# Kernel tuning notes

Measured on AMD Instinct MI355X. Metric: run time of the kernel, lower is better.

## Reference

```python
import jax, jax.numpy as jnp
import numpy as np

N_NODES = 50000
N_EDGES = 800000
IN_CH = 256
OUT_CH = 64
HEADS = 4
NEG_SLOPE = 0.2


def setup_inputs() -> dict:
    key = jax.random.key(0)
    k = jax.random.split(key, 7)
    x = jax.random.normal(k[0], (N_NODES, IN_CH), dtype=jnp.float32)
    edge_index = jax.random.randint(k[1], (2, N_EDGES), 0, N_NODES, dtype=jnp.int32)
    # Glorot-style init for the linear projection and attention vectors
    W = jax.random.normal(k[2], (IN_CH, HEADS * OUT_CH), dtype=jnp.float32) / np.sqrt(IN_CH)
    att_src = jax.random.normal(k[3], (HEADS, OUT_CH), dtype=jnp.float32) / np.sqrt(OUT_CH)
    att_dst = jax.random.normal(k[4], (HEADS, OUT_CH), dtype=jnp.float32) / np.sqrt(OUT_CH)
    bias = jnp.zeros((HEADS * OUT_CH,), dtype=jnp.float32)
    return {"x": x, "edge_index": edge_index, "W": W,
            "att_src": att_src, "att_dst": att_dst, "bias": bias}


def reference(x, edge_index, W, att_src, att_dst, bias):
    N = x.shape[0]
    # PyG GATConv default: add self-loops
    loop = jnp.arange(N, dtype=edge_index.dtype)
    src = jnp.concatenate([edge_index[0], loop])
    dst = jnp.concatenate([edge_index[1], loop])

    h = (x @ W).reshape(N, HEADS, OUT_CH)          # [N,H,C]
    a_src = jnp.einsum('nhc,hc->nh', h, att_src)    # [N,H]
    a_dst = jnp.einsum('nhc,hc->nh', h, att_dst)    # [N,H]

    alpha = a_src[src] + a_dst[dst]                 # [E,H]
    alpha = jax.nn.leaky_relu(alpha, NEG_SLOPE)

    # segment softmax over edges grouped by destination node
    amax = jax.ops.segment_max(alpha, dst, num_segments=N)
    amax = jnp.where(jnp.isfinite(amax), amax, 0.0)
    e = jnp.exp(alpha - amax[dst])
    denom = jax.ops.segment_sum(e, dst, num_segments=N)
    coef = e / (denom[dst] + 1e-16)                 # [E,H]

    msg = coef[..., None] * h[src]                  # [E,H,C]
    out = jax.ops.segment_sum(msg, dst, num_segments=N)  # [N,H,C]
    out = out.reshape(N, HEADS * OUT_CH) + bias
    return jax.nn.relu(out)
```

## Files before the change

kernel.cpp:

```cpp
#include <hip/hip_runtime.h>

#define HC 256
#define NEG_SLOPE 0.2f
#define BM 64
#define BK 64
#define LDK 72

typedef short short8_t __attribute__((ext_vector_type(8)));
typedef float float4_t __attribute__((ext_vector_type(4)));

__device__ __forceinline__ unsigned short f2bf(float f) {
  unsigned u = __float_as_uint(f);
  return (unsigned short)((u + 0x7fffu + ((u >> 16) & 1u)) >> 16);
}
__device__ __forceinline__ float bf2f(unsigned short b) {
  return __uint_as_float(((unsigned)b) << 16);
}

__global__ void wt_kernel(const float* __restrict__ W, unsigned short* __restrict__ Wt)
{
  const int k = blockIdx.x;
  const int n = threadIdx.x;
  Wt[n * 256 + k] = f2bf(W[k * 256 + n]);
}

__global__ __launch_bounds__(256) void gemm_mfma(
    const float* __restrict__ x, const unsigned short* __restrict__ Wt,
    const float* __restrict__ att_src, const float* __restrict__ att_dst,
    unsigned short* __restrict__ h, float* __restrict__ a_src,
    float* __restrict__ a_dst, int nnodes)
{
  __shared__ unsigned short As[BM * LDK];
  __shared__ unsigned short Bs[256 * LDK];
  const int t    = threadIdx.x;
  const int wv   = t >> 6;
  const int lane = t & 63;
  const int r0   = blockIdx.x * BM;

  float4_t acc[4][4] = {};

  for (int k0 = 0; k0 < 256; k0 += BK) {
    __syncthreads();
    {
      const int row = t >> 2, kc = (t & 3) * 16;
      const int gr = r0 + row;
      float4 xv[4];
      if (gr < nnodes) {
        const float4* p = (const float4*)(x + (size_t)gr * 256 + k0 + kc);
        xv[0] = p[0]; xv[1] = p[1]; xv[2] = p[2]; xv[3] = p[3];
      } else {
        xv[0] = xv[1] = xv[2] = xv[3] = make_float4(0.f, 0.f, 0.f, 0.f);
      }
      const float* f = (const float*)xv;
      unsigned pk[8];
      #pragma unroll
      for (int i = 0; i < 8; ++i)
        pk[i] = (unsigned)f2bf(f[2 * i]) | ((unsigned)f2bf(f[2 * i + 1]) << 16);
      uint4* d = (uint4*)&As[row * LDK + kc];
      d[0] = make_uint4(pk[0], pk[1], pk[2], pk[3]);
      d[1] = make_uint4(pk[4], pk[5], pk[6], pk[7]);
    }
    #pragma unroll
    for (int it = 0; it < 4; ++it) {
      const int n = it * 64 + (t >> 2);
      const int kc = (t & 3) * 16;
      const uint4* g = (const uint4*)(Wt + (size_t)n * 256 + k0 + kc);
      uint4 v0 = g[0], v1 = g[1];
      uint4* d = (uint4*)&Bs[n * LDK + kc];
      d[0] = v0; d[1] = v1;
    }
    __syncthreads();

    #pragma unroll
    for (int ks = 0; ks < 2; ++ks) {
      const int ko = ks * 32 + (lane >> 4) * 8;
      short8_t af[4], bfr[4];
      #pragma unroll
      for (int mt = 0; mt < 4; ++mt)
        af[mt] = *(const short8_t*)&As[(16 * mt + (lane & 15)) * LDK + ko];
      #pragma unroll
      for (int nt = 0; nt < 4; ++nt)
        bfr[nt] = *(const short8_t*)&Bs[(64 * wv + 16 * nt + (lane & 15)) * LDK + ko];
      #pragma unroll
      for (int mt = 0; mt < 4; ++mt)
        #pragma unroll
        for (int nt = 0; nt < 4; ++nt)
          acc[mt][nt] = __builtin_amdgcn_mfma_f32_16x16x32_bf16(
              af[mt], bfr[nt], acc[mt][nt], 0, 0, 0);
    }
  }

  const int q = lane >> 4, l15 = lane & 15;
  float atts[4], attd[4];
  #pragma unroll
  for (int nt = 0; nt < 4; ++nt) {
    atts[nt] = att_src[wv * 64 + 16 * nt + l15];
    attd[nt] = att_dst[wv * 64 + 16 * nt + l15];
  }

  #pragma unroll
  for (int mt = 0; mt < 4; ++mt) {
    #pragma unroll
    for (int reg = 0; reg < 4; ++reg) {
      const int row = r0 + 16 * mt + 4 * q + reg;
      const bool ok = row < nnodes;
      float ps = 0.f, pd = 0.f;
      #pragma unroll
      for (int nt = 0; nt < 4; ++nt) {
        const float v = acc[mt][nt][reg];
        if (ok) h[(size_t)row * 256 + 64 * wv + 16 * nt + l15] = f2bf(v);
        ps += v * atts[nt];
        pd += v * attd[nt];
      }
      #pragma unroll
      for (int off = 8; off; off >>= 1) {
        ps += __shfl_down(ps, off, 16);
        pd += __shfl_down(pd, off, 16);
      }
      if (ok && l15 == 0) {
        a_src[row * 4 + wv] = ps;
        a_dst[row * 4 + wv] = pd;
      }
    }
  }
}

__global__ void deg_count(const int* __restrict__ ei, int* __restrict__ deg, int E)
{
  const int e = blockIdx.x * blockDim.x + threadIdx.x;
  if (e >= E) return;
  atomicAdd(&deg[ei[E + e]], 1);
}

__global__ __launch_bounds__(256) void scan_p1(const int* __restrict__ deg,
                                               int* __restrict__ bsum, int n)
{
  __shared__ int ws[4];
  const int t = threadIdx.x, lane = t & 63, wv = t >> 6;
  const int base = blockIdx.x * 1024 + t * 4;
  int4 v = make_int4(0, 0, 0, 0);
  if (base + 3 < n) v = *(const int4*)&deg[base];
  else {
    if (base + 0 < n) v.x = deg[base + 0];
    if (base + 1 < n) v.y = deg[base + 1];
    if (base + 2 < n) v.z = deg[base + 2];
  }
  int s = (v.x + v.y) + (v.z + v.w);
  #pragma unroll
  for (int off = 32; off; off >>= 1) s += __shfl_down(s, off, 64);
  if (lane == 0) ws[wv] = s;
  __syncthreads();
  if (t == 0) bsum[blockIdx.x] = (ws[0] + ws[1]) + (ws[2] + ws[3]);
}

__global__ __launch_bounds__(1024) void scan_p2(const int* __restrict__ bsum,
                                                int* __restrict__ boff,
                                                int* __restrict__ rowptr,
                                                int nb, int n)
{
  __shared__ int wsum[16], woff[16];
  const int t = threadIdx.x, lane = t & 63, wv = t >> 6;
  int v = (t < nb) ? bsum[t] : 0;
  int sc = v;
  #pragma unroll
  for (int off = 1; off < 64; off <<= 1) {
    int u = __shfl_up(sc, off, 64);
    if (lane >= off) sc += u;
  }
  if (lane == 63) wsum[wv] = sc;
  __syncthreads();
  if (t == 0) {
    int run = 0;
    #pragma unroll
    for (int i = 0; i < 16; ++i) { int x = wsum[i]; woff[i] = run; run += x; }
    rowptr[n] = run;
  }
  __syncthreads();
  if (t < nb) boff[t] = woff[wv] + sc - v;
}

__global__ __launch_bounds__(256) void scan_p3(const int* __restrict__ deg,
                                               const int* __restrict__ boff,
                                               int* __restrict__ rowptr,
                                               int* __restrict__ cursor, int n)
{
  __shared__ int wsum[4], woff[4];
  const int t = threadIdx.x, lane = t & 63, wv = t >> 6;
  const int base = blockIdx.x * 1024 + t * 4;
  int4 v = make_int4(0, 0, 0, 0);
  if (base + 3 < n) v = *(const int4*)&deg[base];
  else {
    if (base + 0 < n) v.x = deg[base + 0];
    if (base + 1 < n) v.y = deg[base + 1];
    if (base + 2 < n) v.z = deg[base + 2];
  }
  const int s = (v.x + v.y) + (v.z + v.w);
  int sc = s;
  #pragma unroll
  for (int off = 1; off < 64; off <<= 1) {
    int u = __shfl_up(sc, off, 64);
    if (lane >= off) sc += u;
  }
  if (lane == 63) wsum[wv] = sc;
  __syncthreads();
  if (t == 0) {
    int run = 0;
    #pragma unroll
    for (int i = 0; i < 4; ++i) { int x = wsum[i]; woff[i] = run; run += x; }
  }
  __syncthreads();
  int excl = boff[blockIdx.x] + woff[wv] + (sc - s);
  int4 r;
  r.x = excl;
  r.y = r.x + v.x;
  r.z = r.y + v.y;
  r.w = r.z + v.z;
  if (base + 3 < n) {
    *(int4*)&rowptr[base] = r;
    *(int4*)&cursor[base] = r;
  } else {
    if (base + 0 < n) { rowptr[base + 0] = r.x; cursor[base + 0] = r.x; }
    if (base + 1 < n) { rowptr[base + 1] = r.y; cursor[base + 1] = r.y; }
    if (base + 2 < n) { rowptr[base + 2] = r.z; cursor[base + 2] = r.z; }
  }
}

__global__ void fill_csr(const int* __restrict__ ei, int* __restrict__ cursor,
                         int* __restrict__ csr_src, int E)
{
  const int e = blockIdx.x * blockDim.x + threadIdx.x;
  if (e >= E) return;
  const int d = ei[E + e];
  const int pos = atomicAdd(&cursor[d], 1);
  csr_src[pos] = ei[e];
}

__device__ __forceinline__ float4 ld_h(const unsigned short* __restrict__ h,
                                       int row, int cb)
{
  const ushort4 u = *(const ushort4*)&h[(size_t)row * 256 + cb];
  return make_float4(bf2f(u.x), bf2f(u.y), bf2f(u.z), bf2f(u.w));
}

__global__ __launch_bounds__(256) void gather_kernel(
    const int* __restrict__ rowptr, const int* __restrict__ csr_src,
    const unsigned short* __restrict__ h, const float* __restrict__ a_src,
    const float* __restrict__ a_dst, const float* __restrict__ bias,
    float* __restrict__ out, int n)
{
  const int wave = threadIdx.x >> 6;
  const int lane = threadIdx.x & 63;
  const int d = blockIdx.x * 4 + wave;
  if (d >= n) return;

  const int head = lane >> 4;
  const int cb   = lane * 4;
  const float ad = a_dst[d * 4 + head];

  float alpha = a_src[d * 4 + head] + ad;
  alpha = alpha > 0.f ? alpha : NEG_SLOPE * alpha;
  float w = expf(alpha);
  float dsum = w;
  float4 hv = ld_h(h, d, cb);
  float4 acc = make_float4(w * hv.x, w * hv.y, w * hv.z, w * hv.w);

  int j = rowptr[d];
  const int end = rowptr[d + 1];

  for (; j + 3 < end; j += 4) {
    const int s0 = csr_src[j + 0];
    const int s1 = csr_src[j + 1];
    const int s2 = csr_src[j + 2];
    const int s3 = csr_src[j + 3];
    const float a0 = a_src[s0 * 4 + head];
    const float a1 = a_src[s1 * 4 + head];
    const float a2 = a_src[s2 * 4 + head];
    const float a3 = a_src[s3 * 4 + head];
    const float4 h0 = ld_h(h, s0, cb);
    const float4 h1 = ld_h(h, s1, cb);
    const float4 h2 = ld_h(h, s2, cb);
    const float4 h3 = ld_h(h, s3, cb);
    float l0 = a0 + ad; l0 = l0 > 0.f ? l0 : NEG_SLOPE * l0;
    float l1 = a1 + ad; l1 = l1 > 0.f ? l1 : NEG_SLOPE * l1;
    float l2 = a2 + ad; l2 = l2 > 0.f ? l2 : NEG_SLOPE * l2;
    float l3 = a3 + ad; l3 = l3 > 0.f ? l3 : NEG_SLOPE * l3;
    const float w0 = expf(l0), w1 = expf(l1), w2 = expf(l2), w3 = expf(l3);
    dsum += (w0 + w1) + (w2 + w3);
    acc.x += w0 * h0.x + w1 * h1.x + w2 * h2.x + w3 * h3.x;
    acc.y += w0 * h0.y + w1 * h1.y + w2 * h2.y + w3 * h3.y;
    acc.z += w0 * h0.z + w1 * h1.z + w2 * h2.z + w3 * h3.z;
    acc.w += w0 * h0.w + w1 * h1.w + w2 * h2.w + w3 * h3.w;
  }
  for (; j < end; ++j) {
    const int s0 = csr_src[j];
    const float a0 = a_src[s0 * 4 + head];
    const float4 h0 = ld_h(h, s0, cb);
    float l0 = a0 + ad; l0 = l0 > 0.f ? l0 : NEG_SLOPE * l0;
    const float w0 = expf(l0);
    dsum += w0;
    acc.x += w0 * h0.x; acc.y += w0 * h0.y;
    acc.z += w0 * h0.z; acc.w += w0 * h0.w;
  }

  const float inv = 1.f / (dsum + 1e-16f);
  const float4 b4 = ((const float4*)bias)[lane];
  float4 o;
  o.x = acc.x * inv + b4.x; o.x = o.x > 0.f ? o.x : 0.f;
  o.y = acc.y * inv + b4.y; o.y = o.y > 0.f ? o.y : 0.f;
  o.z = acc.z * inv + b4.z; o.z = o.z > 0.f ? o.z : 0.f;
  o.w = acc.w * inv + b4.w; o.w = o.w > 0.f ? o.w : 0.f;
  *(float4*)&out[(size_t)d * 256 + cb] = o;
}

extern "C" void kernel_launch(void* const* d_in, const int* in_sizes, int n_in,
                              void* d_out, int out_size, void* d_ws, size_t ws_size,
                              hipStream_t stream)
{
  const float* x       = (const float*)d_in[0];
  const int*   ei      = (const int*)d_in[1];
  const float* W       = (const float*)d_in[2];
  const float* att_src = (const float*)d_in[3];
  const float* att_dst = (const float*)d_in[4];
  const float* bias    = (const float*)d_in[5];

  const int nnodes = in_sizes[0] / HC;
  const int E      = in_sizes[1] / 2;
  const int nb     = (nnodes + 1023) / 1024;

  float* out = (float*)d_out;
  char* ws = (char*)d_ws;
  unsigned short* h  = (unsigned short*)ws;
  float* a_src = (float*)(ws + (size_t)nnodes * HC * 2);
  float* a_dst = a_src + (size_t)nnodes * 4;
  unsigned short* Wt = (unsigned short*)(a_dst + (size_t)nnodes * 4);
  int* deg    = (int*)((char*)Wt + 256 * 256 * 2);
  int* rowptr = deg + nnodes;
  int* cursor = rowptr + ((nnodes + 1 + 3) & ~3);
  int* bsum   = cursor + nnodes;
  int* boff   = bsum + ((nb + 3) & ~3);
  int* csr    = boff + ((nb + 3) & ~3);

  hipMemsetAsync(deg, 0, (size_t)nnodes * sizeof(int), stream);

  wt_kernel<<<256, 256, 0, stream>>>(W, Wt);

  gemm_mfma<<<(nnodes + BM - 1) / BM, 256, 0, stream>>>(
      x, Wt, att_src, att_dst, h, a_src, a_dst, nnodes);

  deg_count<<<(E + 255) / 256, 256, 0, stream>>>(ei, deg, E);
  scan_p1<<<nb, 256, 0, stream>>>(deg, bsum, nnodes);
  scan_p2<<<1, 1024, 0, stream>>>(bsum, boff, rowptr, nb, nnodes);
  scan_p3<<<nb, 256, 0, stream>>>(deg, boff, rowptr, cursor, nnodes);
  fill_csr<<<(E + 255) / 256, 256, 0, stream>>>(ei, cursor, csr, E);

  gather_kernel<<<(nnodes + 3) / 4, 256, 0, stream>>>(
      rowptr, csr, h, a_src, a_dst, bias, out, nnodes);
}
```

Baseline: 297.0 us.

## Precompute per-edge attention exponentials during CSR fill and partition by destination range

The CSR fill kernel now also computes leaky-ReLU plus exp of the attention logits for all four heads of each edge and stores them in a new per-edge float4 buffer. The gather kernel then reads these weights instead of gathering a_src and recomputing exp. Fill_csr is restructured into 8 destination-range groups over a fixed grid of 1024 blocks, so each group's atomics and cursor updates stay in a narrower address range. The catch is that every group rescans the whole destination array and an extra per-edge buffer is written and read. The x-to-bf16 pack in the GEMM also switches to the packed bf16x2 conversion intrinsic.

```diff
diff --git a/kernel.cpp b/kernel.cpp
--- a/kernel.cpp
+++ b/kernel.cpp
@@ -1,4 +1,5 @@
 #include <hip/hip_runtime.h>
+#include <hip/hip_bf16.h>
 
 #define HC 256
 #define NEG_SLOPE 0.2f
@@ -54,8 +55,10 @@
       const float* f = (const float*)xv;
       unsigned pk[8];
       #pragma unroll
-      for (int i = 0; i < 8; ++i)
-        pk[i] = (unsigned)f2bf(f[2 * i]) | ((unsigned)f2bf(f[2 * i + 1]) << 16);
+      for (int i = 0; i < 8; ++i) {
+        __hip_bfloat162 b2 = __float22bfloat162_rn(make_float2(f[2 * i], f[2 * i + 1]));
+        pk[i] = *(unsigned*)&b2;
+      }
       uint4* d = (uint4*)&As[row * LDK + kc];
       d[0] = make_uint4(pk[0], pk[1], pk[2], pk[3]);
       d[1] = make_uint4(pk[4], pk[5], pk[6], pk[7]);
@@ -225,14 +228,36 @@
   }
 }
 
-__global__ void fill_csr(const int* __restrict__ ei, int* __restrict__ cursor,
-                         int* __restrict__ csr_src, int E)
-{
-  const int e = blockIdx.x * blockDim.x + threadIdx.x;
-  if (e >= E) return;
-  const int d = ei[E + e];
-  const int pos = atomicAdd(&cursor[d], 1);
-  csr_src[pos] = ei[e];
+__global__ __launch_bounds__(256) void fill_csr(
+    const int* __restrict__ ei, const float* __restrict__ a_src,
+    const float* __restrict__ a_dst, int* __restrict__ cursor,
+    int* __restrict__ csr_src, float4* __restrict__ wexp, int E, int nnodes)
+{
+  const int g    = blockIdx.x & 7;
+  const int bg   = blockIdx.x >> 3;
+  const int nbg  = gridDim.x >> 3;
+  const int gsz  = (nnodes + 7) >> 3;
+  const int dlo  = g * gsz;
+  const int dhi  = min(dlo + gsz, nnodes);
+
+  for (int e = bg * 256 + threadIdx.x; e < E; e += nbg * 256) {
+    const int d = ei[E + e];
+    if (d < dlo || d >= dhi) continue;
+    const int s = ei[e];
+    const int pos = atomicAdd(&cursor[d], 1);
+    csr_src[pos] = s;
+    const float4 as = ((const float4*)a_src)[s];
+    const float4 ad = ((const float4*)a_dst)[d];
+    float4 al;
+    al.x = as.x + ad.x; al.y = as.y + ad.y;
+    al.z = as.z + ad.z; al.w = as.w + ad.w;
+    al.x = al.x > 0.f ? al.x : NEG_SLOPE * al.x;
+    al.y = al.y > 0.f ? al.y : NEG_SLOPE * al.y;
+    al.z = al.z > 0.f ? al.z : NEG_SLOPE * al.z;
+    al.w = al.w > 0.f ? al.w : NEG_SLOPE * al.w;
+    al.x = expf(al.x); al.y = expf(al.y); al.z = expf(al.z); al.w = expf(al.w);
+    wexp[pos] = al;
+  }
 }
 
 __device__ __forceinline__ float4 ld_h(const unsigned short* __restrict__ h,
@@ -244,9 +269,9 @@
 
 __global__ __launch_bounds__(256) void gather_kernel(
     const int* __restrict__ rowptr, const int* __restrict__ csr_src,
-    const unsigned short* __restrict__ h, const float* __restrict__ a_src,
-    const float* __restrict__ a_dst, const float* __restrict__ bias,
-    float* __restrict__ out, int n)
+    const float* __restrict__ wexp, const unsigned short* __restrict__ h,
+    const float* __restrict__ a_src, const float* __restrict__ a_dst,
+    const float* __restrict__ bias, float* __restrict__ out, int n)
 {
   const int wave = threadIdx.x >> 6;
   const int lane = threadIdx.x & 63;
@@ -255,9 +280,8 @@
 
   const int head = lane >> 4;
   const int cb   = lane * 4;
-  const float ad = a_dst[d * 4 + head];
-
-  float alpha = a_src[d * 4 + head] + ad;
+
+  float alpha = a_src[d * 4 + head] + a_dst[d * 4 + head];
   alpha = alpha > 0.f ? alpha : NEG_SLOPE * alpha;
   float w = expf(alpha);
   float dsum = w;
@@ -268,23 +292,15 @@
   const int end = rowptr[d + 1];
 
   for (; j + 3 < end; j += 4) {
-    const int s0 = csr_src[j + 0];
-    const int s1 = csr_src[j + 1];
-    const int s2 = csr_src[j + 2];
-    const int s3 = csr_src[j + 3];
-    const float a0 = a_src[s0 * 4 + head];
-    const float a1 = a_src[s1 * 4 + head];
-    const float a2 = a_src[s2 * 4 + head];
-    const float a3 = a_src[s3 * 4 + head];
-    const float4 h0 = ld_h(h, s0, cb);
-    const float4 h1 = ld_h(h, s1, cb);
-    const float4 h2 = ld_h(h, s2, cb);
-    const float4 h3 = ld_h(h, s3, cb);
-    float l0 = a0 + ad; l0 = l0 > 0.f ? l0 : NEG_SLOPE * l0;
-    float l1 = a1 + ad; l1 = l1 > 0.f ? l1 : NEG_SLOPE * l1;
-    float l2 = a2 + ad; l2 = l2 > 0.f ? l2 : NEG_SLOPE * l2;
-    float l3 = a3 + ad; l3 = l3 > 0.f ? l3 : NEG_SLOPE * l3;
-    const float w0 = expf(l0), w1 = expf(l1), w2 = expf(l2), w3 = expf(l3);
+    const int4 s4 = *(const int4*)&csr_src[j];
+    const float w0 = wexp[(j + 0) * 4 + head];
+    const float w1 = wexp[(j + 1) * 4 + head];
+    const float w2 = wexp[(j + 2) * 4 + head];
+    const float w3 = wexp[(j + 3) * 4 + head];
+    const float4 h0 = ld_h(h, s4.x, cb);
+    const float4 h1 = ld_h(h, s4.y, cb);
+    const float4 h2 = ld_h(h, s4.z, cb);
+    const float4 h3 = ld_h(h, s4.w, cb);
     dsum += (w0 + w1) + (w2 + w3);
     acc.x += w0 * h0.x + w1 * h1.x + w2 * h2.x + w3 * h3.x;
     acc.y += w0 * h0.y + w1 * h1.y + w2 * h2.y + w3 * h3.y;
@@ -293,10 +309,8 @@
   }
   for (; j < end; ++j) {
     const int s0 = csr_src[j];
-    const float a0 = a_src[s0 * 4 + head];
+    const float w0 = wexp[j * 4 + head];
     const float4 h0 = ld_h(h, s0, cb);
-    float l0 = a0 + ad; l0 = l0 > 0.f ? l0 : NEG_SLOPE * l0;
-    const float w0 = expf(l0);
     dsum += w0;
     acc.x += w0 * h0.x; acc.y += w0 * h0.y;
     acc.z += w0 * h0.z; acc.w += w0 * h0.w;
@@ -338,7 +352,8 @@
   int* cursor = rowptr + ((nnodes + 1 + 3) & ~3);
   int* bsum   = cursor + nnodes;
   int* boff   = bsum + ((nb + 3) & ~3);
-  int* csr    = boff + ((nb + 3) & ~3);
+  float4* wexp = (float4*)(boff + ((nb + 3) & ~3));
+  int* csr    = (int*)(wexp + E);
 
   hipMemsetAsync(deg, 0, (size_t)nnodes * sizeof(int), stream);
 
@@ -351,8 +366,10 @@
   scan_p1<<<nb, 256, 0, stream>>>(deg, bsum, nnodes);
   scan_p2<<<1, 1024, 0, stream>>>(bsum, boff, rowptr, nb, nnodes);
   scan_p3<<<nb, 256, 0, stream>>>(deg, boff, rowptr, cursor, nnodes);
-  fill_csr<<<(E + 255) / 256, 256, 0, stream>>>(ei, cursor, csr, E);
+
+  fill_csr<<<1024, 256, 0, stream>>>(ei, a_src, a_dst, cursor, csr,
+                                     (float4*)wexp, E, nnodes);
 
   gather_kernel<<<(nnodes + 3) / 4, 256, 0, stream>>>(
-      rowptr, csr, h, a_src, a_dst, bias, out, nnodes);
-}
+      rowptr, csr, (const float*)wexp, h, a_src, a_dst, bias, out, nnodes);
+}
```

After: 276.7 us. 1.07x faster.
